# Kernel optimization log

Measured on AMD Instinct MI355X. Metric: run time of the kernel, lower is better.

Reference implementation:

```python
import jax, jax.numpy as jnp
import numpy as np

N_NODES = 100000
N_EDGES = 3200000
F_IN, F_HID, F_OUT = 61, 16, 2  # num_features, hidden, num_classes
K = 2  # kernel_size (dim=1, degree=1 linear open B-spline)


def spline_conv(x, src, dst, u, W, root, bias, n_nodes):
    """SplineConv, dim=1, kernel_size=2, degree=1, open spline, aggr='mean'.
    Linear B-spline basis on u in [0,1]: B0 = 1-u, B1 = u.
    Since the basis depends only on the edge and the transform is linear,
    precompute both node-level transforms then gather+blend per edge.
    W: [K, f_in, f_out], root: [f_in, f_out], bias: [f_out].
    """
    h = jnp.einsum('nf,kfc->knc', x, W)  # [K, N, f_out] (tiny matmuls)
    w1 = u[:, 0]            # [E]
    w0 = 1.0 - w1
    msg = w0[:, None] * h[0][src] + w1[:, None] * h[1][src]  # [E, f_out]
    summed = jax.ops.segment_sum(msg, dst, num_segments=n_nodes)
    cnt = jax.ops.segment_sum(jnp.ones((msg.shape[0],), msg.dtype), dst,
                              num_segments=n_nodes)
    out = summed / jnp.maximum(cnt, 1.0)[:, None]            # mean aggregation
    return out + x @ root + bias


def setup_inputs() -> dict:
    key = jax.random.key(0)
    ks = jax.random.split(key, 9)
    x = jax.random.normal(ks[0], (N_NODES, F_IN), dtype=jnp.float32)
    edge_index = jax.random.randint(ks[1], (2, N_EDGES), 0, N_NODES, dtype=jnp.int64)
    edge_attr = jax.random.uniform(ks[2], (N_EDGES, 1), dtype=jnp.float32)
    s1 = 1.0 / np.sqrt(F_IN)
    s2 = 1.0 / np.sqrt(F_HID)
    W1 = jax.random.normal(ks[3], (K, F_IN, F_HID), dtype=jnp.float32) * s1
    root1 = jax.random.normal(ks[4], (F_IN, F_HID), dtype=jnp.float32) * s1
    b1 = jnp.zeros((F_HID,), jnp.float32)
    W2 = jax.random.normal(ks[5], (K, F_HID, F_OUT), dtype=jnp.float32) * s2
    root2 = jax.random.normal(ks[6], (F_HID, F_OUT), dtype=jnp.float32) * s2
    b2 = jnp.zeros((F_OUT,), jnp.float32)
    return {"x": x, "edge_index": edge_index, "edge_attr": edge_attr,
            "dropout": 0, "W1": W1, "root1": root1, "b1": b1,
            "W2": W2, "root2": root2, "b2": b2}


def reference(x, edge_index, edge_attr, dropout, W1, root1, b1, W2, root2, b2):
    # Eval mode: F.dropout(training=False) is identity; `dropout` arg is unused
    # in the original forward body.
    src, dst = edge_index[0], edge_index[1]
    n = x.shape[0]
    h = spline_conv(x, src, dst, edge_attr, W1, root1, b1, n)
    h = jax.nn.elu(h)
    h = spline_conv(h, src, dst, edge_attr, W2, root2, b2, n)
    return jax.nn.log_softmax(h, axis=1)
```

## Files before the change

### kernel.cpp

```cpp
#include <hip/hip_runtime.h>
#include <hip/hip_fp16.h>

#define N_NODES 100000
#define N_EDGES 3200000
#define F_IN    61
#define F_HID   16
#define F_OUT   2
#define HB      256
#define CHUNK   (N_EDGES / HB)
#define BSIZE   512
#define NBUCK   196

typedef unsigned int uint;

__global__ __launch_bounds__(128) void k_transform1(
    const float* __restrict__ x, const float* __restrict__ W1,
    const float* __restrict__ root1, const float* __restrict__ b1,
    __half2* __restrict__ hp, float* __restrict__ r1)
{
    __shared__ float xs[128 * F_IN];
    __shared__ float w0s[F_IN * F_HID];
    __shared__ float w1s[F_IN * F_HID];
    __shared__ float rs [F_IN * F_HID];
    __shared__ float bs [F_HID];

    const int tid = threadIdx.x;
    for (int i = tid; i < F_IN * F_HID; i += 128) {
        w0s[i] = W1[i];
        w1s[i] = W1[F_IN * F_HID + i];
        rs[i]  = root1[i];
    }
    if (tid < F_HID) bs[tid] = b1[tid];

    const int n0 = blockIdx.x * 128;
    const int nodes = min(128, N_NODES - n0);
    for (int i = tid; i < nodes * F_IN; i += 128)
        xs[i] = x[(size_t)n0 * F_IN + i];
    __syncthreads();

    if (tid < nodes) {
        const int n = n0 + tid;
        float a0[F_HID], a1[F_HID], ar[F_HID];
        #pragma unroll
        for (int c = 0; c < F_HID; ++c) { a0[c] = 0.f; a1[c] = 0.f; ar[c] = 0.f; }
        const float* xr = &xs[tid * F_IN];
        for (int f = 0; f < F_IN; ++f) {
            const float xv = xr[f];
            #pragma unroll
            for (int c = 0; c < F_HID; ++c) {
                a0[c] = fmaf(xv, w0s[f * F_HID + c], a0[c]);
                a1[c] = fmaf(xv, w1s[f * F_HID + c], a1[c]);
                ar[c] = fmaf(xv, rs [f * F_HID + c], ar[c]);
            }
        }
        #pragma unroll
        for (int c = 0; c < F_HID; ++c) {
            hp[(size_t)n * F_HID + c] = __floats2half2_rn(a0[c], a1[c]);
            r1[(size_t)n * F_HID + c] = ar[c] + bs[c];
        }
    }
}

__global__ __launch_bounds__(1024) void k_bhist(
    const int* __restrict__ edst, uint* __restrict__ cnt)
{
    __shared__ uint bins[NBUCK];
    const int bx = blockIdx.x, tid = threadIdx.x;
    for (int i = tid; i < NBUCK; i += 1024) bins[i] = 0;
    __syncthreads();
    const int e0 = bx * CHUNK, e1 = e0 + CHUNK;
    for (int e = e0 + tid; e < e1; e += 1024)
        atomicAdd(&bins[((uint)edst[e]) >> 9], 1u);
    __syncthreads();
    for (int i = tid; i < NBUCK; i += 1024) cnt[(size_t)i * HB + bx] = bins[i];
}

__global__ __launch_bounds__(256) void k_brow1(
    uint* __restrict__ cnt, uint* __restrict__ tot)
{
    __shared__ uint s[256];
    const int b = blockIdx.x, tid = threadIdx.x;
    const uint v = cnt[(size_t)b * HB + tid];
    s[tid] = v; __syncthreads();
    for (int off = 1; off < 256; off <<= 1) {
        const uint t = (tid >= off) ? s[tid - off] : 0u;
        __syncthreads();
        s[tid] += t;
        __syncthreads();
    }
    cnt[(size_t)b * HB + tid] = s[tid] - v;
    if (tid == 255) tot[b] = s[255];
}

__global__ __launch_bounds__(256) void k_bexc(
    const uint* __restrict__ tot, uint* __restrict__ bstart)
{
    __shared__ uint s[256];
    const int tid = threadIdx.x;
    const uint v = (tid < NBUCK) ? tot[tid] : 0u;
    s[tid] = v; __syncthreads();
    for (int off = 1; off < 256; off <<= 1) {
        const uint t = (tid >= off) ? s[tid - off] : 0u;
        __syncthreads();
        s[tid] += t;
        __syncthreads();
    }
    if (tid < NBUCK) bstart[tid] = s[tid] - v;
    if (tid == 0) bstart[NBUCK] = N_EDGES;
}

__global__ __launch_bounds__(1024) void k_bscatter(
    const int* __restrict__ esrc, const int* __restrict__ edst,
    const float* __restrict__ attr, const uint* __restrict__ cnt,
    const uint* __restrict__ bstart, uint2* __restrict__ buck)
{
    __shared__ uint pos[NBUCK];
    const int bx = blockIdx.x, tid = threadIdx.x;
    for (int i = tid; i < NBUCK; i += 1024)
        pos[i] = cnt[(size_t)i * HB + bx] + bstart[i];
    __syncthreads();
    const int e0 = bx * CHUNK, e1 = e0 + CHUNK;
    for (int e = e0 + tid; e < e1; e += 1024) {
        const uint d = (uint)edst[e];
        const uint p = atomicAdd(&pos[d >> 9], 1u);
        buck[p] = make_uint2((uint)esrc[e] | ((d & 511u) << 17),
                             __float_as_uint(attr[e]));
    }
}

__global__ __launch_bounds__(1024) void k_fscatter(
    const uint2* __restrict__ buck, const uint* __restrict__ bstart,
    uint* __restrict__ rowptr, uint* __restrict__ vals)
{
    __shared__ uint deg[BSIZE];
    __shared__ uint excl[BSIZE];
    const int b = blockIdx.x, tid = threadIdx.x;
    const uint e0 = bstart[b], e1 = bstart[b + 1];

    for (int i = tid; i < BSIZE; i += 1024) deg[i] = 0;
    __syncthreads();
    for (uint e = e0 + tid; e < e1; e += 1024)
        atomicAdd(&deg[(buck[e].x >> 17) & 511u], 1u);
    __syncthreads();

    if (tid < BSIZE) excl[tid] = deg[tid];
    __syncthreads();
    for (int off = 1; off < BSIZE; off <<= 1) {
        uint t = 0;
        if (tid < BSIZE && tid >= off) t = excl[tid - off];
        __syncthreads();
        if (tid < BSIZE) excl[tid] += t;
        __syncthreads();
    }
    if (tid < BSIZE) {
        const uint ex = excl[tid] - deg[tid];
        const int n = b * BSIZE + tid;
        if (n < N_NODES) rowptr[n] = e0 + ex;
        deg[tid] = ex;
    }
    if (b == 0 && tid == 0) rowptr[N_NODES] = N_EDGES;
    __syncthreads();

    for (uint e = e0 + tid; e < e1; e += 1024) {
        const uint2 w = buck[e];
        const uint dl = (w.x >> 17) & 511u;
        const uint p = atomicAdd(&deg[dl], 1u);
        const float uf = __uint_as_float(w.y);
        const uint uq = (uint)(uf * 32767.0f + 0.5f);
        vals[e0 + p] = ((w.x & 0x1FFFFu) << 15) | uq;
    }
}

__global__ __launch_bounds__(256) void k_agg1(
    const uint* __restrict__ rowptr, const uint* __restrict__ vals,
    const uint2* __restrict__ hp2, float2* __restrict__ sum1)
{
    __shared__ uint ent[4][64];
    const int tid = threadIdx.x;
    const int lane = tid & 63;
    const int wave = tid >> 6;
    const int n = blockIdx.x * 4 + wave;
    const int ep = lane >> 3;
    const int q  = lane & 7;

    const uint r0 = rowptr[n];
    const uint deg = rowptr[n + 1] - r0;
    const uint dcap = min(deg, 64u);

    if ((uint)lane < dcap)
        ent[wave][lane] = __builtin_nontemporal_load(&vals[r0 + lane]);
    __syncthreads();

    __half2 acc_a = __float2half2_rn(0.f);
    __half2 acc_b = __float2half2_rn(0.f);
    #pragma unroll 4
    for (uint i = ep; i < dcap; i += 8) {
        const uint v  = ent[wave][i];
        const float uu = (float)(v & 32767u) * (1.0f / 32767.0f);
        const __half2 wv = __floats2half2_rn(1.0f - uu, uu);
        const uint2 hw = hp2[(size_t)(v >> 15) * 8 + q];
        acc_a = __hfma2(wv, *(const __half2*)&hw.x, acc_a);
        acc_b = __hfma2(wv, *(const __half2*)&hw.y, acc_b);
    }
    for (uint i = 64 + ep; i < deg; i += 8) {
        const uint v  = __builtin_nontemporal_load(&vals[r0 + i]);
        const float uu = (float)(v & 32767u) * (1.0f / 32767.0f);
        const __half2 wv = __floats2half2_rn(1.0f - uu, uu);
        const uint2 hw = hp2[(size_t)(v >> 15) * 8 + q];
        acc_a = __hfma2(wv, *(const __half2*)&hw.x, acc_a);
        acc_b = __hfma2(wv, *(const __half2*)&hw.y, acc_b);
    }
    const float2 fa = __half22float2(acc_a);
    const float2 fb = __half22float2(acc_b);
    float a0 = fa.x + fa.y;
    float a1 = fb.x + fb.y;
    a0 += __shfl_xor(a0, 8); a0 += __shfl_xor(a0, 16); a0 += __shfl_xor(a0, 32);
    a1 += __shfl_xor(a1, 8); a1 += __shfl_xor(a1, 16); a1 += __shfl_xor(a1, 32);

    if (lane < 8)
        sum1[(size_t)n * 8 + lane] = make_float2(a0, a1);
}

__global__ __launch_bounds__(256) void k_mid2(
    const float2* __restrict__ sum1, const uint* __restrict__ rowptr,
    const float* __restrict__ r1,
    const float* __restrict__ W2, const float* __restrict__ root2,
    const float* __restrict__ b2,
    float4* __restrict__ h2, float2* __restrict__ r2)
{
    __shared__ float w2s[2 * F_HID * F_OUT];
    __shared__ float rts[F_HID * F_OUT];
    __shared__ float b2s[F_OUT];
    const int tid = threadIdx.x;
    if (tid < 2 * F_HID * F_OUT) w2s[tid] = W2[tid];
    if (tid < F_HID * F_OUT)     rts[tid] = root2[tid];
    if (tid < F_OUT)             b2s[tid] = b2[tid];
    __syncthreads();

    const int n = blockIdx.x * 256 + tid;
    if (n >= N_NODES) return;

    const uint deg = rowptr[n + 1] - rowptr[n];
    const float inv = 1.0f / (float)max(deg, 1u);

    float h[F_HID];
    #pragma unroll
    for (int k = 0; k < 8; ++k) {
        const float2 s = sum1[(size_t)n * 8 + k];
        const float v0 = s.x * inv + r1[(size_t)n * F_HID + 2 * k];
        const float v1 = s.y * inv + r1[(size_t)n * F_HID + 2 * k + 1];
        h[2 * k]     = (v0 > 0.0f) ? v0 : expm1f(v0);
        h[2 * k + 1] = (v1 > 0.0f) ? v1 : expm1f(v1);
    }
    float o00 = 0.f, o01 = 0.f, o10 = 0.f, o11 = 0.f;
    float rr0 = b2s[0], rr1 = b2s[1];
    #pragma unroll
    for (int f = 0; f < F_HID; ++f) {
        o00 = fmaf(h[f], w2s[f * 2 + 0], o00);
        o01 = fmaf(h[f], w2s[f * 2 + 1], o01);
        o10 = fmaf(h[f], w2s[2 * F_HID + f * 2 + 0], o10);
        o11 = fmaf(h[f], w2s[2 * F_HID + f * 2 + 1], o11);
        rr0 = fmaf(h[f], rts[f * 2 + 0], rr0);
        rr1 = fmaf(h[f], rts[f * 2 + 1], rr1);
    }
    h2[n] = make_float4(o00, o10, o01, o11);
    r2[n] = make_float2(rr0, rr1);
}

__global__ __launch_bounds__(256) void k_agg2(
    const uint* __restrict__ rowptr, const uint* __restrict__ vals,
    const float2* __restrict__ h2f2, const float2* __restrict__ r2,
    float* __restrict__ out)
{
    __shared__ uint ent[4][64];
    const int tid = threadIdx.x;
    const int lane = tid & 63;
    const int wave = tid >> 6;
    const int n = blockIdx.x * 4 + wave;
    const int ep = lane >> 1;
    const int fp = lane & 1;

    const uint r0 = rowptr[n];
    const uint deg = rowptr[n + 1] - r0;
    const uint dcap = min(deg, 64u);

    if ((uint)lane < dcap)
        ent[wave][lane] = __builtin_nontemporal_load(&vals[r0 + lane]);
    __syncthreads();

    float acc = 0.f;
    #pragma unroll 2
    for (uint i = ep; i < dcap; i += 32) {
        const uint v  = ent[wave][i];
        const float uu = (float)(v & 32767u) * (1.0f / 32767.0f);
        const float2 g = h2f2[(size_t)(v >> 15) * 2 + fp];
        acc += (1.0f - uu) * g.x + uu * g.y;
    }
    for (uint i = 64 + ep; i < deg; i += 32) {
        const uint v  = __builtin_nontemporal_load(&vals[r0 + i]);
        const float uu = (float)(v & 32767u) * (1.0f / 32767.0f);
        const float2 g = h2f2[(size_t)(v >> 15) * 2 + fp];
        acc += (1.0f - uu) * g.x + uu * g.y;
    }
    #pragma unroll
    for (int off = 2; off < 64; off <<= 1) acc += __shfl_xor(acc, off);

    const float inv = 1.0f / (float)max(deg, 1u);
    const float rv = fp ? r2[n].y : r2[n].x;
    const float o = acc * inv + rv;
    const float other = __shfl_xor(o, 1);
    const float m = fmaxf(o, other);
    const float l = m + logf(expf(o - m) + expf(other - m));
    if (lane < 2) out[(size_t)n * 2 + fp] = o - l;
}

extern "C" void kernel_launch(void* const* d_in, const int* in_sizes, int n_in,
                              void* d_out, int out_size, void* d_ws, size_t ws_size,
                              hipStream_t stream) {
    const float* x     = (const float*)d_in[0];
    const int*   ei    = (const int*)  d_in[1];
    const float* attr  = (const float*)d_in[2];
    const float* W1    = (const float*)d_in[4];
    const float* root1 = (const float*)d_in[5];
    const float* b1    = (const float*)d_in[6];
    const float* W2    = (const float*)d_in[7];
    const float* root2 = (const float*)d_in[8];
    const float* b2    = (const float*)d_in[9];
    float* out = (float*)d_out;

    char* ws = (char*)d_ws;
    size_t off = 0;
    uint*  vals   = (uint*) (ws + off); off += (size_t)N_EDGES * sizeof(uint);
    uint*  rowptr = (uint*) (ws + off); off += (size_t)(N_NODES + 1) * sizeof(uint);
    uint*  cnt    = (uint*) (ws + off); off += (size_t)NBUCK * HB * sizeof(uint);
    uint*  bstart = (uint*) (ws + off); off += (size_t)(NBUCK + 1) * sizeof(uint);
    uint*  tot    = (uint*) (ws + off); off += (size_t)NBUCK * sizeof(uint);
    off = (off + 255) & ~(size_t)255;
    uint2* buck   = (uint2*)(ws + off); off += (size_t)N_EDGES * sizeof(uint2);

    char* alias = (char*)buck;
    size_t aoff = 0;
    __half2* hp = (__half2*)(alias + aoff); aoff += (size_t)N_NODES * F_HID * sizeof(__half2);
    float*   r1 = (float*)  (alias + aoff); aoff += (size_t)N_NODES * F_HID * sizeof(float);
    float4*  h2 = (float4*) (alias + aoff); aoff += (size_t)N_NODES * sizeof(float4);
    float2*  r2 = (float2*) (alias + aoff); aoff += (size_t)N_NODES * sizeof(float2);
    float2* sum1= (float2*) (alias + aoff); aoff += (size_t)N_NODES * 8 * sizeof(float2);
    (void)ws_size;

    const int* esrc = ei;
    const int* edst = ei + N_EDGES;

    k_bhist    <<<HB, 1024, 0, stream>>>(edst, cnt);
    k_brow1    <<<NBUCK, 256, 0, stream>>>(cnt, tot);
    k_bexc     <<<1, 256, 0, stream>>>(tot, bstart);
    k_bscatter <<<HB, 1024, 0, stream>>>(esrc, edst, attr, cnt, bstart, buck);
    k_fscatter <<<NBUCK, 1024, 0, stream>>>(buck, bstart, rowptr, vals);
    k_transform1<<<(N_NODES + 127) / 128, 128, 0, stream>>>(x, W1, root1, b1, hp, r1);
    k_agg1     <<<N_NODES / 4, 256, 0, stream>>>(rowptr, vals, (const uint2*)hp, sum1);
    k_mid2     <<<(N_NODES + 255) / 256, 256, 0, stream>>>(sum1, rowptr, r1, W2, root2, b2, h2, r2);
    k_agg2     <<<N_NODES / 4, 256, 0, stream>>>(rowptr, vals, (const float2*)h2, r2, out);
}
```

Baseline: 189.2 us.

## Fuse CSR fine-scatter, layer-1 aggregation and mid transform into one bucket kernel

Shrinks buckets from 512 to 128 destination nodes (782 buckets) so each bucket's edges fit in a shared-memory buffer. A single kernel now builds the per-bucket CSR, keeps the packed entries in LDS, aggregates layer-1 messages from LDS, and applies ELU plus the layer-2 transform. This removes the separate fscatter, agg1 and mid2 launches along with the sum1 round trip and the re-read of vals. Risks: fewer, heavier blocks with large LDS use lower occupancy, and buckets that overflow CAP fall back to a slower global path. The histogram kernel also splits its bins into two copies to reduce atomic contention.

```diff
diff --git a/kernel.cpp b/kernel.cpp
--- a/kernel.cpp
+++ b/kernel.cpp
@@ -8,8 +8,10 @@
 #define F_OUT   2
 #define HB      256
 #define CHUNK   (N_EDGES / HB)
-#define BSIZE   512
-#define NBUCK   196
+#define BSIZE   128
+#define NBUCK   782
+#define CAP     5120
+#define RPT     (CAP / 512)
 
 typedef unsigned int uint;
 
@@ -64,15 +66,18 @@
 __global__ __launch_bounds__(1024) void k_bhist(
     const int* __restrict__ edst, uint* __restrict__ cnt)
 {
-    __shared__ uint bins[NBUCK];
+    __shared__ uint bins[2][NBUCK];
+    uint* fb = &bins[0][0];
     const int bx = blockIdx.x, tid = threadIdx.x;
-    for (int i = tid; i < NBUCK; i += 1024) bins[i] = 0;
+    for (int i = tid; i < 2 * NBUCK; i += 1024) fb[i] = 0;
     __syncthreads();
     const int e0 = bx * CHUNK, e1 = e0 + CHUNK;
+    const int sb = tid & 1;
     for (int e = e0 + tid; e < e1; e += 1024)
-        atomicAdd(&bins[((uint)edst[e]) >> 9], 1u);
-    __syncthreads();
-    for (int i = tid; i < NBUCK; i += 1024) cnt[(size_t)i * HB + bx] = bins[i];
+        atomicAdd(&bins[sb][((uint)edst[e]) >> 7], 1u);
+    __syncthreads();
+    for (int i = tid; i < NBUCK; i += 1024)
+        cnt[(size_t)i * HB + bx] = bins[0][i] + bins[1][i];
 }
 
 __global__ __launch_bounds__(256) void k_brow1(
@@ -92,14 +97,14 @@
     if (tid == 255) tot[b] = s[255];
 }
 
-__global__ __launch_bounds__(256) void k_bexc(
+__global__ __launch_bounds__(1024) void k_bexc(
     const uint* __restrict__ tot, uint* __restrict__ bstart)
 {
-    __shared__ uint s[256];
+    __shared__ uint s[1024];
     const int tid = threadIdx.x;
     const uint v = (tid < NBUCK) ? tot[tid] : 0u;
     s[tid] = v; __syncthreads();
-    for (int off = 1; off < 256; off <<= 1) {
+    for (int off = 1; off < 1024; off <<= 1) {
         const uint t = (tid >= off) ? s[tid - off] : 0u;
         __syncthreads();
         s[tid] += t;
@@ -122,25 +127,54 @@
     const int e0 = bx * CHUNK, e1 = e0 + CHUNK;
     for (int e = e0 + tid; e < e1; e += 1024) {
         const uint d = (uint)edst[e];
-        const uint p = atomicAdd(&pos[d >> 9], 1u);
-        buck[p] = make_uint2((uint)esrc[e] | ((d & 511u) << 17),
+        const uint p = atomicAdd(&pos[d >> 7], 1u);
+        buck[p] = make_uint2((uint)esrc[e] | ((d & 127u) << 17),
                              __float_as_uint(attr[e]));
     }
 }
 
-__global__ __launch_bounds__(1024) void k_fscatter(
+__global__ __launch_bounds__(512) void k_fagg1(
     const uint2* __restrict__ buck, const uint* __restrict__ bstart,
-    uint* __restrict__ rowptr, uint* __restrict__ vals)
-{
-    __shared__ uint deg[BSIZE];
-    __shared__ uint excl[BSIZE];
+    const uint2* __restrict__ hp2, const float* __restrict__ r1,
+    const float* __restrict__ W2, const float* __restrict__ root2,
+    const float* __restrict__ b2,
+    uint* __restrict__ rowptr, uint* __restrict__ vals,
+    float4* __restrict__ h2, float2* __restrict__ r2)
+{
+    __shared__ uint  ent[CAP];
+    __shared__ uint  deg[BSIZE], excl[BSIZE], pos[BSIZE];
+    __shared__ float sums[F_HID][BSIZE];
+    __shared__ float w2s[2 * F_HID * F_OUT];
+    __shared__ float rts[F_HID * F_OUT];
+    __shared__ float b2s[F_OUT];
+
     const int b = blockIdx.x, tid = threadIdx.x;
     const uint e0 = bstart[b], e1 = bstart[b + 1];
-
-    for (int i = tid; i < BSIZE; i += 1024) deg[i] = 0;
-    __syncthreads();
-    for (uint e = e0 + tid; e < e1; e += 1024)
-        atomicAdd(&deg[(buck[e].x >> 17) & 511u], 1u);
+    const uint seg = e1 - e0;
+    const bool fits = (seg <= (uint)CAP);
+
+    if (tid < 2 * F_HID * F_OUT) w2s[tid] = W2[tid];
+    if (tid < F_HID * F_OUT)     rts[tid] = root2[tid];
+    if (tid < F_OUT)             b2s[tid] = b2[tid];
+    if (tid < BSIZE) deg[tid] = 0;
+    __syncthreads();
+
+    uint2 r[RPT];
+    if (fits) {
+        #pragma unroll
+        for (int k = 0; k < RPT; ++k) {
+            const uint e = e0 + (uint)tid + (uint)k * 512u;
+            if (e < e1) r[k] = buck[e];
+        }
+        #pragma unroll
+        for (int k = 0; k < RPT; ++k) {
+            const uint e = e0 + (uint)tid + (uint)k * 512u;
+            if (e < e1) atomicAdd(&deg[(r[k].x >> 17) & 127u], 1u);
+        }
+    } else {
+        for (uint e = e0 + tid; e < e1; e += 512)
+            atomicAdd(&deg[(buck[e].x >> 17) & 127u], 1u);
+    }
     __syncthreads();
 
     if (tid < BSIZE) excl[tid] = deg[tid];
@@ -154,117 +188,107 @@
     }
     if (tid < BSIZE) {
         const uint ex = excl[tid] - deg[tid];
+        excl[tid] = ex;
+        pos[tid]  = ex;
         const int n = b * BSIZE + tid;
         if (n < N_NODES) rowptr[n] = e0 + ex;
-        deg[tid] = ex;
     }
     if (b == 0 && tid == 0) rowptr[N_NODES] = N_EDGES;
     __syncthreads();
 
-    for (uint e = e0 + tid; e < e1; e += 1024) {
-        const uint2 w = buck[e];
-        const uint dl = (w.x >> 17) & 511u;
-        const uint p = atomicAdd(&deg[dl], 1u);
-        const float uf = __uint_as_float(w.y);
-        const uint uq = (uint)(uf * 32767.0f + 0.5f);
-        vals[e0 + p] = ((w.x & 0x1FFFFu) << 15) | uq;
-    }
-}
-
-__global__ __launch_bounds__(256) void k_agg1(
-    const uint* __restrict__ rowptr, const uint* __restrict__ vals,
-    const uint2* __restrict__ hp2, float2* __restrict__ sum1)
-{
-    __shared__ uint ent[4][64];
-    const int tid = threadIdx.x;
+    if (fits) {
+        #pragma unroll
+        for (int k = 0; k < RPT; ++k) {
+            const uint e = e0 + (uint)tid + (uint)k * 512u;
+            if (e < e1) {
+                const uint dl = (r[k].x >> 17) & 127u;
+                const uint p  = atomicAdd(&pos[dl], 1u);
+                const float uf = __uint_as_float(r[k].y);
+                const uint uq = (uint)(uf * 32767.0f + 0.5f);
+                const uint pk = ((r[k].x & 0x1FFFFu) << 15) | uq;
+                ent[p] = pk;
+                vals[e0 + p] = pk;
+            }
+        }
+    } else {
+        for (uint e = e0 + tid; e < e1; e += 512) {
+            const uint2 w = buck[e];
+            const uint dl = (w.x >> 17) & 127u;
+            const uint p  = atomicAdd(&pos[dl], 1u);
+            const float uf = __uint_as_float(w.y);
+            const uint uq = (uint)(uf * 32767.0f + 0.5f);
+            vals[e0 + p] = ((w.x & 0x1FFFFu) << 15) | uq;
+        }
+    }
+    __syncthreads();
+
+    const int wave = tid >> 6;
     const int lane = tid & 63;
-    const int wave = tid >> 6;
-    const int n = blockIdx.x * 4 + wave;
     const int ep = lane >> 3;
     const int q  = lane & 7;
 
-    const uint r0 = rowptr[n];
-    const uint deg = rowptr[n + 1] - r0;
-    const uint dcap = min(deg, 64u);
-
-    if ((uint)lane < dcap)
-        ent[wave][lane] = __builtin_nontemporal_load(&vals[r0 + lane]);
-    __syncthreads();
-
-    __half2 acc_a = __float2half2_rn(0.f);
-    __half2 acc_b = __float2half2_rn(0.f);
-    #pragma unroll 4
-    for (uint i = ep; i < dcap; i += 8) {
-        const uint v  = ent[wave][i];
-        const float uu = (float)(v & 32767u) * (1.0f / 32767.0f);
-        const __half2 wv = __floats2half2_rn(1.0f - uu, uu);
-        const uint2 hw = hp2[(size_t)(v >> 15) * 8 + q];
-        acc_a = __hfma2(wv, *(const __half2*)&hw.x, acc_a);
-        acc_b = __hfma2(wv, *(const __half2*)&hw.y, acc_b);
-    }
-    for (uint i = 64 + ep; i < deg; i += 8) {
-        const uint v  = __builtin_nontemporal_load(&vals[r0 + i]);
-        const float uu = (float)(v & 32767u) * (1.0f / 32767.0f);
-        const __half2 wv = __floats2half2_rn(1.0f - uu, uu);
-        const uint2 hw = hp2[(size_t)(v >> 15) * 8 + q];
-        acc_a = __hfma2(wv, *(const __half2*)&hw.x, acc_a);
-        acc_b = __hfma2(wv, *(const __half2*)&hw.y, acc_b);
-    }
-    const float2 fa = __half22float2(acc_a);
-    const float2 fb = __half22float2(acc_b);
-    float a0 = fa.x + fa.y;
-    float a1 = fb.x + fb.y;
-    a0 += __shfl_xor(a0, 8); a0 += __shfl_xor(a0, 16); a0 += __shfl_xor(a0, 32);
-    a1 += __shfl_xor(a1, 8); a1 += __shfl_xor(a1, 16); a1 += __shfl_xor(a1, 32);
-
-    if (lane < 8)
-        sum1[(size_t)n * 8 + lane] = make_float2(a0, a1);
-}
-
-__global__ __launch_bounds__(256) void k_mid2(
-    const float2* __restrict__ sum1, const uint* __restrict__ rowptr,
-    const float* __restrict__ r1,
-    const float* __restrict__ W2, const float* __restrict__ root2,
-    const float* __restrict__ b2,
-    float4* __restrict__ h2, float2* __restrict__ r2)
-{
-    __shared__ float w2s[2 * F_HID * F_OUT];
-    __shared__ float rts[F_HID * F_OUT];
-    __shared__ float b2s[F_OUT];
-    const int tid = threadIdx.x;
-    if (tid < 2 * F_HID * F_OUT) w2s[tid] = W2[tid];
-    if (tid < F_HID * F_OUT)     rts[tid] = root2[tid];
-    if (tid < F_OUT)             b2s[tid] = b2[tid];
-    __syncthreads();
-
-    const int n = blockIdx.x * 256 + tid;
-    if (n >= N_NODES) return;
-
-    const uint deg = rowptr[n + 1] - rowptr[n];
-    const float inv = 1.0f / (float)max(deg, 1u);
-
-    float h[F_HID];
-    #pragma unroll
-    for (int k = 0; k < 8; ++k) {
-        const float2 s = sum1[(size_t)n * 8 + k];
-        const float v0 = s.x * inv + r1[(size_t)n * F_HID + 2 * k];
-        const float v1 = s.y * inv + r1[(size_t)n * F_HID + 2 * k + 1];
-        h[2 * k]     = (v0 > 0.0f) ? v0 : expm1f(v0);
-        h[2 * k + 1] = (v1 > 0.0f) ? v1 : expm1f(v1);
-    }
-    float o00 = 0.f, o01 = 0.f, o10 = 0.f, o11 = 0.f;
-    float rr0 = b2s[0], rr1 = b2s[1];
-    #pragma unroll
-    for (int f = 0; f < F_HID; ++f) {
-        o00 = fmaf(h[f], w2s[f * 2 + 0], o00);
-        o01 = fmaf(h[f], w2s[f * 2 + 1], o01);
-        o10 = fmaf(h[f], w2s[2 * F_HID + f * 2 + 0], o10);
-        o11 = fmaf(h[f], w2s[2 * F_HID + f * 2 + 1], o11);
-        rr0 = fmaf(h[f], rts[f * 2 + 0], rr0);
-        rr1 = fmaf(h[f], rts[f * 2 + 1], rr1);
-    }
-    h2[n] = make_float4(o00, o10, o01, o11);
-    r2[n] = make_float2(rr0, rr1);
+#define AGG_LOOP(READ_EXPR)                                                    \
+    for (int j = 0; j < BSIZE / 8; ++j) {                                      \
+        const int nl = wave * (BSIZE / 8) + j;                                 \
+        const uint start = excl[nl];                                           \
+        const uint dg = deg[nl];                                               \
+        __half2 acc_a = __floats2half2_rn(0.f, 0.f);                           \
+        __half2 acc_b = __floats2half2_rn(0.f, 0.f);                           \
+        _Pragma("unroll 4")                                                    \
+        for (uint i = ep; i < dg; i += 8) {                                    \
+            const uint v = (READ_EXPR);                                        \
+            const float uu = (float)(v & 32767u) * (1.0f / 32767.0f);          \
+            const __half2 wv = __floats2half2_rn(1.0f - uu, uu);               \
+            const uint2 hw = hp2[(size_t)(v >> 15) * 8 + q];                   \
+            acc_a = __hfma2(wv, *(const __half2*)&hw.x, acc_a);                \
+            acc_b = __hfma2(wv, *(const __half2*)&hw.y, acc_b);                \
+        }                                                                      \
+        const float2 fa = __half22float2(acc_a);                               \
+        const float2 fb = __half22float2(acc_b);                               \
+        float a0 = fa.x + fa.y, a1 = fb.x + fb.y;                              \
+        a0 += __shfl_xor(a0, 8); a0 += __shfl_xor(a0, 16); a0 += __shfl_xor(a0, 32); \
+        a1 += __shfl_xor(a1, 8); a1 += __shfl_xor(a1, 16); a1 += __shfl_xor(a1, 32); \
+        if (lane < 8) { sums[2 * lane][nl] = a0; sums[2 * lane + 1][nl] = a1; } \
+    }
+
+    if (fits) { AGG_LOOP(ent[start + i]) }
+    else      { AGG_LOOP(vals[e0 + start + i]) }
+#undef AGG_LOOP
+    __syncthreads();
+
+    if (tid < BSIZE) {
+        const int n = b * BSIZE + tid;
+        if (n < N_NODES) {
+            const float inv = 1.0f / (float)max(deg[tid], 1u);
+            float h[F_HID];
+            const float4* r1v = (const float4*)(r1 + (size_t)n * F_HID);
+            #pragma unroll
+            for (int k4 = 0; k4 < 4; ++k4) {
+                const float4 rv = r1v[k4];
+                const float v0 = sums[4 * k4 + 0][tid] * inv + rv.x;
+                const float v1 = sums[4 * k4 + 1][tid] * inv + rv.y;
+                const float v2 = sums[4 * k4 + 2][tid] * inv + rv.z;
+                const float v3 = sums[4 * k4 + 3][tid] * inv + rv.w;
+                h[4 * k4 + 0] = (v0 > 0.0f) ? v0 : expm1f(v0);
+                h[4 * k4 + 1] = (v1 > 0.0f) ? v1 : expm1f(v1);
+                h[4 * k4 + 2] = (v2 > 0.0f) ? v2 : expm1f(v2);
+                h[4 * k4 + 3] = (v3 > 0.0f) ? v3 : expm1f(v3);
+            }
+            float o00 = 0.f, o01 = 0.f, o10 = 0.f, o11 = 0.f;
+            float rr0 = b2s[0], rr1 = b2s[1];
+            #pragma unroll
+            for (int f = 0; f < F_HID; ++f) {
+                o00 = fmaf(h[f], w2s[f * 2 + 0], o00);
+                o01 = fmaf(h[f], w2s[f * 2 + 1], o01);
+                o10 = fmaf(h[f], w2s[2 * F_HID + f * 2 + 0], o10);
+                o11 = fmaf(h[f], w2s[2 * F_HID + f * 2 + 1], o11);
+                rr0 = fmaf(h[f], rts[f * 2 + 0], rr0);
+                rr1 = fmaf(h[f], rts[f * 2 + 1], rr1);
+            }
+            h2[n] = make_float4(o00, o10, o01, o11);
+            r2[n] = make_float2(rr0, rr1);
+        }
+    }
 }
 
 __global__ __launch_bounds__(256) void k_agg2(
@@ -330,33 +354,28 @@
 
     char* ws = (char*)d_ws;
     size_t off = 0;
-    uint*  vals   = (uint*) (ws + off); off += (size_t)N_EDGES * sizeof(uint);
-    uint*  rowptr = (uint*) (ws + off); off += (size_t)(N_NODES + 1) * sizeof(uint);
-    uint*  cnt    = (uint*) (ws + off); off += (size_t)NBUCK * HB * sizeof(uint);
-    uint*  bstart = (uint*) (ws + off); off += (size_t)(NBUCK + 1) * sizeof(uint);
-    uint*  tot    = (uint*) (ws + off); off += (size_t)NBUCK * sizeof(uint);
+    uint2*   buck  = (uint2*)  (ws + off); off += (size_t)N_EDGES * sizeof(uint2);
+    uint*    vals  = (uint*)   (ws + off); off += (size_t)N_EDGES * sizeof(uint);
+    uint*    rowptr= (uint*)   (ws + off); off += (size_t)(N_NODES + 1) * sizeof(uint);
+    uint*    cnt   = (uint*)   (ws + off); off += (size_t)NBUCK * HB * sizeof(uint);
+    uint*    bstart= (uint*)   (ws + off); off += (size_t)(NBUCK + 1) * sizeof(uint);
+    uint*    tot   = (uint*)   (ws + off); off += (size_t)NBUCK * sizeof(uint);
     off = (off + 255) & ~(size_t)255;
-    uint2* buck   = (uint2*)(ws + off); off += (size_t)N_EDGES * sizeof(uint2);
-
-    char* alias = (char*)buck;
-    size_t aoff = 0;
-    __half2* hp = (__half2*)(alias + aoff); aoff += (size_t)N_NODES * F_HID * sizeof(__half2);
-    float*   r1 = (float*)  (alias + aoff); aoff += (size_t)N_NODES * F_HID * sizeof(float);
-    float4*  h2 = (float4*) (alias + aoff); aoff += (size_t)N_NODES * sizeof(float4);
-    float2*  r2 = (float2*) (alias + aoff); aoff += (size_t)N_NODES * sizeof(float2);
-    float2* sum1= (float2*) (alias + aoff); aoff += (size_t)N_NODES * 8 * sizeof(float2);
+    __half2* hp    = (__half2*)(ws + off); off += (size_t)N_NODES * F_HID * sizeof(__half2);
+    float*   r1    = (float*)  (ws + off); off += (size_t)N_NODES * F_HID * sizeof(float);
+    float4*  h2    = (float4*) (ws + off); off += (size_t)N_NODES * sizeof(float4);
+    float2*  r2    = (float2*) (ws + off); off += (size_t)N_NODES * sizeof(float2);
     (void)ws_size;
 
     const int* esrc = ei;
     const int* edst = ei + N_EDGES;
 
-    k_bhist    <<<HB, 1024, 0, stream>>>(edst, cnt);
-    k_brow1    <<<NBUCK, 256, 0, stream>>>(cnt, tot);
-    k_bexc     <<<1, 256, 0, stream>>>(tot, bstart);
-    k_bscatter <<<HB, 1024, 0, stream>>>(esrc, edst, attr, cnt, bstart, buck);
-    k_fscatter <<<NBUCK, 1024, 0, stream>>>(buck, bstart, rowptr, vals);
+    k_bhist     <<<HB, 1024, 0, stream>>>(edst, cnt);
+    k_brow1     <<<NBUCK, 256, 0, stream>>>(cnt, tot);
+    k_bexc      <<<1, 1024, 0, stream>>>(tot, bstart);
+    k_bscatter  <<<HB, 1024, 0, stream>>>(esrc, edst, attr, cnt, bstart, buck);
     k_transform1<<<(N_NODES + 127) / 128, 128, 0, stream>>>(x, W1, root1, b1, hp, r1);
-    k_agg1     <<<N_NODES / 4, 256, 0, stream>>>(rowptr, vals, (const uint2*)hp, sum1);
-    k_mid2     <<<(N_NODES + 255) / 256, 256, 0, stream>>>(sum1, rowptr, r1, W2, root2, b2, h2, r2);
-    k_agg2     <<<N_NODES / 4, 256, 0, stream>>>(rowptr, vals, (const float2*)h2, r2, out);
-}
+    k_fagg1     <<<NBUCK, 512, 0, stream>>>(buck, bstart, (const uint2*)hp, r1,
+                                            W2, root2, b2, rowptr, vals, h2, r2);
+    k_agg2      <<<N_NODES / 4, 256, 0, stream>>>(rowptr, vals, (const float2*)h2, r2, out);
+}
```

After: 190.4 us. No clear change (+0.6%).

## Split layer-1 gather table into two feature halves aggregated in separate passes

Applied to the files above, without the earlier changes.

The fp16 node table used by the first aggregation is split into two 3.2 MB halves, each holding 8 of the 16 hidden channels. The aggregation kernel runs twice, once per half, with 16 edges per wave in flight. The aim is for each pass's random-gather working set to fit better in cache (L2/MALL), at the cost of reading the CSR index array twice and launching one more kernel.

```diff
diff --git a/kernel.cpp b/kernel.cpp
--- a/kernel.cpp
+++ b/kernel.cpp
@@ -16,7 +16,8 @@
 __global__ __launch_bounds__(128) void k_transform1(
     const float* __restrict__ x, const float* __restrict__ W1,
     const float* __restrict__ root1, const float* __restrict__ b1,
-    __half2* __restrict__ hp, float* __restrict__ r1)
+    __half2* __restrict__ hpA, __half2* __restrict__ hpB,
+    float* __restrict__ r1)
 {
     __shared__ float xs[128 * F_IN];
     __shared__ float w0s[F_IN * F_HID];
@@ -54,10 +55,14 @@
             }
         }
         #pragma unroll
-        for (int c = 0; c < F_HID; ++c) {
-            hp[(size_t)n * F_HID + c] = __floats2half2_rn(a0[c], a1[c]);
+        for (int c = 0; c < 8; ++c)
+            hpA[(size_t)n * 8 + c] = __floats2half2_rn(a0[c], a1[c]);
+        #pragma unroll
+        for (int c = 0; c < 8; ++c)
+            hpB[(size_t)n * 8 + c] = __floats2half2_rn(a0[8 + c], a1[8 + c]);
+        #pragma unroll
+        for (int c = 0; c < F_HID; ++c)
             r1[(size_t)n * F_HID + c] = ar[c] + bs[c];
-        }
     }
 }
 
@@ -171,17 +176,17 @@
     }
 }
 
-__global__ __launch_bounds__(256) void k_agg1(
+__global__ __launch_bounds__(256) void k_agg1h(
     const uint* __restrict__ rowptr, const uint* __restrict__ vals,
-    const uint2* __restrict__ hp2, float2* __restrict__ sum1)
+    const uint2* __restrict__ tab, float2* __restrict__ sumb)
 {
     __shared__ uint ent[4][64];
     const int tid = threadIdx.x;
     const int lane = tid & 63;
     const int wave = tid >> 6;
     const int n = blockIdx.x * 4 + wave;
-    const int ep = lane >> 3;
-    const int q  = lane & 7;
+    const int ep = lane >> 2;
+    const int q  = lane & 3;
 
     const uint r0 = rowptr[n];
     const uint deg = rowptr[n + 1] - r0;
@@ -194,19 +199,19 @@
     __half2 acc_a = __float2half2_rn(0.f);
     __half2 acc_b = __float2half2_rn(0.f);
     #pragma unroll 4
-    for (uint i = ep; i < dcap; i += 8) {
+    for (uint i = ep; i < dcap; i += 16) {
         const uint v  = ent[wave][i];
         const float uu = (float)(v & 32767u) * (1.0f / 32767.0f);
         const __half2 wv = __floats2half2_rn(1.0f - uu, uu);
-        const uint2 hw = hp2[(size_t)(v >> 15) * 8 + q];
+        const uint2 hw = tab[(size_t)(v >> 15) * 4 + q];
         acc_a = __hfma2(wv, *(const __half2*)&hw.x, acc_a);
         acc_b = __hfma2(wv, *(const __half2*)&hw.y, acc_b);
     }
-    for (uint i = 64 + ep; i < deg; i += 8) {
+    for (uint i = 64 + ep; i < deg; i += 16) {
         const uint v  = __builtin_nontemporal_load(&vals[r0 + i]);
         const float uu = (float)(v & 32767u) * (1.0f / 32767.0f);
         const __half2 wv = __floats2half2_rn(1.0f - uu, uu);
-        const uint2 hw = hp2[(size_t)(v >> 15) * 8 + q];
+        const uint2 hw = tab[(size_t)(v >> 15) * 4 + q];
         acc_a = __hfma2(wv, *(const __half2*)&hw.x, acc_a);
         acc_b = __hfma2(wv, *(const __half2*)&hw.y, acc_b);
     }
@@ -214,11 +219,13 @@
     const float2 fb = __half22float2(acc_b);
     float a0 = fa.x + fa.y;
     float a1 = fb.x + fb.y;
-    a0 += __shfl_xor(a0, 8); a0 += __shfl_xor(a0, 16); a0 += __shfl_xor(a0, 32);
-    a1 += __shfl_xor(a1, 8); a1 += __shfl_xor(a1, 16); a1 += __shfl_xor(a1, 32);
-
-    if (lane < 8)
-        sum1[(size_t)n * 8 + lane] = make_float2(a0, a1);
+    a0 += __shfl_xor(a0, 4); a0 += __shfl_xor(a0, 8);
+    a0 += __shfl_xor(a0, 16); a0 += __shfl_xor(a0, 32);
+    a1 += __shfl_xor(a1, 4); a1 += __shfl_xor(a1, 8);
+    a1 += __shfl_xor(a1, 16); a1 += __shfl_xor(a1, 32);
+
+    if (lane < 4)
+        sumb[(size_t)n * 8 + lane] = make_float2(a0, a1);
 }
 
 __global__ __launch_bounds__(256) void k_mid2(
@@ -340,11 +347,12 @@
 
     char* alias = (char*)buck;
     size_t aoff = 0;
-    __half2* hp = (__half2*)(alias + aoff); aoff += (size_t)N_NODES * F_HID * sizeof(__half2);
-    float*   r1 = (float*)  (alias + aoff); aoff += (size_t)N_NODES * F_HID * sizeof(float);
-    float4*  h2 = (float4*) (alias + aoff); aoff += (size_t)N_NODES * sizeof(float4);
-    float2*  r2 = (float2*) (alias + aoff); aoff += (size_t)N_NODES * sizeof(float2);
-    float2* sum1= (float2*) (alias + aoff); aoff += (size_t)N_NODES * 8 * sizeof(float2);
+    __half2* hpA = (__half2*)(alias + aoff); aoff += (size_t)N_NODES * 8 * sizeof(__half2);
+    __half2* hpB = (__half2*)(alias + aoff); aoff += (size_t)N_NODES * 8 * sizeof(__half2);
+    float*   r1  = (float*)  (alias + aoff); aoff += (size_t)N_NODES * F_HID * sizeof(float);
+    float4*  h2  = (float4*) (alias + aoff); aoff += (size_t)N_NODES * sizeof(float4);
+    float2*  r2  = (float2*) (alias + aoff); aoff += (size_t)N_NODES * sizeof(float2);
+    float2* sum1 = (float2*) (alias + aoff); aoff += (size_t)N_NODES * 8 * sizeof(float2);
     (void)ws_size;
 
     const int* esrc = ei;
@@ -355,8 +363,9 @@
     k_bexc     <<<1, 256, 0, stream>>>(tot, bstart);
     k_bscatter <<<HB, 1024, 0, stream>>>(esrc, edst, attr, cnt, bstart, buck);
     k_fscatter <<<NBUCK, 1024, 0, stream>>>(buck, bstart, rowptr, vals);
-    k_transform1<<<(N_NODES + 127) / 128, 128, 0, stream>>>(x, W1, root1, b1, hp, r1);
-    k_agg1     <<<N_NODES / 4, 256, 0, stream>>>(rowptr, vals, (const uint2*)hp, sum1);
+    k_transform1<<<(N_NODES + 127) / 128, 128, 0, stream>>>(x, W1, root1, b1, hpA, hpB, r1);
+    k_agg1h    <<<N_NODES / 4, 256, 0, stream>>>(rowptr, vals, (const uint2*)hpA, sum1);
+    k_agg1h    <<<N_NODES / 4, 256, 0, stream>>>(rowptr, vals, (const uint2*)hpB, sum1 + 4);
     k_mid2     <<<(N_NODES + 255) / 256, 256, 0, stream>>>(sum1, rowptr, r1, W2, root2, b2, h2, r2);
     k_agg2     <<<N_NODES / 4, 256, 0, stream>>>(rowptr, vals, (const float2*)h2, r2, out);
 }
```

Measured after the change: 216.6 us. 14.5% more time.
